# Kernel optimization log

Measured on AMD Instinct MI355X. Metric: run time of the kernel, lower is better.

The kernel has to match this reference:

```python
import jax, jax.numpy as jnp
import numpy as np
import math

B, L, D = 4, 4096, 1024
M = 256  # num random features
EPS = 1e-06


def setup_inputs() -> dict:
    key = jax.random.key(0)
    kq, kk, kv, kp = jax.random.split(key, 4)
    Q = jax.random.normal(kq, (B, L, D), dtype=jnp.float32)
    K = jax.random.normal(kk, (B, L, D), dtype=jnp.float32)
    V = jax.random.normal(kv, (B, L, D), dtype=jnp.float32)
    # Gaussian random projection (ortho_features=False path): shape (num_features, d_model)
    projection = jax.random.normal(kp, (M, D), dtype=jnp.float32)
    return {"Q": Q, "K": K, "V": V, "projection": projection}


def reference(Q, K, V, projection):
    d_model = Q.shape[-1]
    m = projection.shape[0]
    inv_sqrt_d = 1.0 / math.sqrt(d_model)
    # random features: exp((x / sqrt(d)) @ P^T)
    rf_q = jnp.exp(jnp.einsum('bld,md->blm', Q * inv_sqrt_d, projection)) / math.sqrt(m)  # (B,L,M)
    rf_k = jnp.exp(jnp.einsum('bld,md->blm', K * inv_sqrt_d, projection))                 # (B,L,M)
    # linear attention: KV state and normalizer
    KV = jnp.einsum('blm,bld->bmd', rf_k, V)   # (B,M,D)
    Z = jnp.sum(rf_k, axis=1)                   # (B,M)
    out = jnp.einsum('blm,bmd->bld', rf_q, KV)  # (B,L,D)
    normalizer = jnp.einsum('blm,bm->bl', rf_q, Z) + EPS  # (B,L)
    return out / normalizer[..., None]
```

## Files before the change

kernel.cpp:

```cpp
#include <hip/hip_runtime.h>
#include <math.h>

#define NB 4
#define LL 4096
#define DD 1024
#define MM 256

typedef short s16x8 __attribute__((ext_vector_type(8)));
typedef short s16x4 __attribute__((ext_vector_type(4)));
typedef float fx4 __attribute__((ext_vector_type(4)));
typedef unsigned u32x2 __attribute__((ext_vector_type(2)));
typedef unsigned u32x4 __attribute__((ext_vector_type(4)));

__device__ __forceinline__ float b2f(short s) {
  union { unsigned u; float f; } v;
  v.u = ((unsigned)(unsigned short)s) << 16;
  return v.f;
}
__device__ __forceinline__ short f2b(float f) {
  union { float f; unsigned u; } v;
  v.f = f;
  unsigned r = (v.u + 0x7fffu + ((v.u >> 16) & 1u)) >> 16;
  return (short)(unsigned short)r;
}
__device__ __forceinline__ unsigned cvt2(float lo, float hi) {
  unsigned r;
  asm("v_cvt_pk_bf16_f32 %0, %1, %2" : "=v"(r) : "v"(lo), "v"(hi));
  return r;
}
__device__ __forceinline__ int swz(int row, int col) {
  return row * 64 + (col ^ ((row & 7) << 3));
}
__device__ __forceinline__ int keyf(int m) { return (m ^ (m >> 2)) & 3; }

typedef __attribute__((address_space(1))) const void* gas1_t;
typedef __attribute__((address_space(3))) void* las3_t;
#define GLL16(g, l) __builtin_amdgcn_global_load_lds((gas1_t)(const void*)(g), (las3_t)(void*)(l), 16, 0, 0)

__global__ __launch_bounds__(256) void k_cast(const float* __restrict__ in, short* __restrict__ out, int n4) {
  int i = blockIdx.x * 256 + threadIdx.x;
  if (i >= n4) return;
  float4 v = ((const float4*)in)[i];
  s16x4 s;
  s[0] = f2b(v.x); s[1] = f2b(v.y); s[2] = f2b(v.z); s[3] = f2b(v.w);
  ((s16x4*)out)[i] = s;
}

__global__ __launch_bounds__(256, 2) void k_qk(const float* __restrict__ Q, const float* __restrict__ K,
                                               const short* __restrict__ Pb,
                                               short* __restrict__ rfq, short* __restrict__ rfkT,
                                               float* __restrict__ Zz) {
  __shared__ short As[2][8192];
  __shared__ short Bs[2][8192];
  int z = blockIdx.z, mode = z >> 2, b = z & 3;
  int m0 = blockIdx.x * 128, l0 = blockIdx.y * 128;
  const float* X = mode ? K : Q;
  int tid = threadIdx.x, lane = tid & 63, w = tid >> 6;
  int wr = w >> 1, wc = w & 1;
  int m16 = lane & 15, kg = lane >> 4;

  int arow = tid >> 1, acolh = (tid & 1) * 32;
  int akey = (arow & 7) << 3;
  const float* Xr = X + ((size_t)b * LL + l0 + arow) * DD + acolh;
  const short* PbB = Pb + (size_t)m0 * DD;

  fx4 acc[4][4] = {};
  float4 pa[8];

  #pragma unroll
  for (int i = 0; i < 8; ++i) pa[i] = *(const float4*)(Xr + i * 4);
  #pragma unroll
  for (int j = 0; j < 4; ++j) {
    int fl = tid + j * 256, row = fl >> 3, c8 = fl & 7;
    GLL16(PbB + (size_t)row * DD + (c8 ^ (row & 7)) * 8, &Bs[0][fl * 8]);
  }
  #pragma unroll
  for (int i = 0; i < 4; ++i) {
    u32x4 vv;
    vv[0] = cvt2(pa[2 * i].x, pa[2 * i].y);
    vv[1] = cvt2(pa[2 * i].z, pa[2 * i].w);
    vv[2] = cvt2(pa[2 * i + 1].x, pa[2 * i + 1].y);
    vv[3] = cvt2(pa[2 * i + 1].z, pa[2 * i + 1].w);
    *(u32x4*)&As[0][arow * 64 + ((acolh + i * 8) ^ akey)] = vv;
  }
  __syncthreads();

  for (int t = 0; t < 16; ++t) {
    int cur = t & 1, nxt = cur ^ 1;
    if (t < 15) {
      int d1 = (t + 1) * 64;
      #pragma unroll
      for (int i = 0; i < 8; ++i) pa[i] = *(const float4*)(Xr + d1 + i * 4);
      #pragma unroll
      for (int j = 0; j < 4; ++j) {
        int fl = tid + j * 256, row = fl >> 3, c8 = fl & 7;
        GLL16(PbB + (size_t)row * DD + d1 + (c8 ^ (row & 7)) * 8, &Bs[nxt][fl * 8]);
      }
    }
    #pragma unroll
    for (int ks = 0; ks < 2; ++ks) {
      int kb = ks * 32 + kg * 8;
      s16x8 af[4], bf[4];
      #pragma unroll
      for (int mi = 0; mi < 4; ++mi) af[mi] = *(const s16x8*)&As[cur][swz(wr * 64 + mi * 16 + m16, kb)];
      #pragma unroll
      for (int ni = 0; ni < 4; ++ni) bf[ni] = *(const s16x8*)&Bs[cur][swz(wc * 64 + ni * 16 + m16, kb)];
      #pragma unroll
      for (int mi = 0; mi < 4; ++mi)
        #pragma unroll
        for (int ni = 0; ni < 4; ++ni)
          acc[mi][ni] = __builtin_amdgcn_mfma_f32_16x16x32_bf16(af[mi], bf[ni], acc[mi][ni], 0, 0, 0);
    }
    if (t < 15) {
      #pragma unroll
      for (int i = 0; i < 4; ++i) {
        u32x4 vv;
        vv[0] = cvt2(pa[2 * i].x, pa[2 * i].y);
        vv[1] = cvt2(pa[2 * i].z, pa[2 * i].w);
        vv[2] = cvt2(pa[2 * i + 1].x, pa[2 * i + 1].y);
        vv[3] = cvt2(pa[2 * i + 1].z, pa[2 * i + 1].w);
        *(u32x4*)&As[nxt][arow * 64 + ((acolh + i * 8) ^ akey)] = vv;
      }
    }
    __syncthreads();
  }

  if (mode == 0) {
    #pragma unroll
    for (int mi = 0; mi < 4; ++mi)
      #pragma unroll
      for (int ni = 0; ni < 4; ++ni) {
        int r0 = wr * 64 + mi * 16 + (kg << 2);
        int c = m0 + wc * 64 + ni * 16 + m16;
        #pragma unroll
        for (int u = 0; u < 4; ++u)
          rfq[((size_t)b * LL + l0 + r0 + u) * MM + c] = f2b(expf(acc[mi][ni][u] * 0.03125f) * 0.0625f);
      }
  } else {
    short* T = (short*)As;
    float zp[4] = {0.f, 0.f, 0.f, 0.f};
    #pragma unroll
    for (int mi = 0; mi < 4; ++mi)
      #pragma unroll
      for (int ni = 0; ni < 4; ++ni) {
        int l = wr * 64 + mi * 16 + (kg << 2);
        int m = wc * 64 + ni * 16 + m16;
        int key = (m & 7) << 3;
        float e0 = expf(acc[mi][ni][0] * 0.03125f);
        float e1 = expf(acc[mi][ni][1] * 0.03125f);
        float e2 = expf(acc[mi][ni][2] * 0.03125f);
        float e3 = expf(acc[mi][ni][3] * 0.03125f);
        zp[ni] += e0 + e1 + e2 + e3;
        *(unsigned*)&T[m * 128 + (l ^ key)] = cvt2(e0, e1);
        *(unsigned*)&T[m * 128 + ((l + 2) ^ key)] = cvt2(e2, e3);
      }
    #pragma unroll
    for (int ni = 0; ni < 4; ++ni) {
      zp[ni] += __shfl_xor(zp[ni], 16);
      zp[ni] += __shfl_xor(zp[ni], 32);
    }
    if (kg == 0) {
      #pragma unroll
      for (int ni = 0; ni < 4; ++ni)
        atomicAdd(&Zz[b * MM + m0 + wc * 64 + ni * 16 + m16], zp[ni]);
    }
    __syncthreads();
    int m = tid >> 1, lh = (tid & 1) * 64;
    int mkey = (m & 7) << 3;
    short* dst = rfkT + ((size_t)b * MM + m0 + m) * LL + l0 + lh;
    #pragma unroll
    for (int j = 0; j < 8; ++j) {
      int l = lh + j * 8;
      s16x8 v = *(const s16x8*)&T[m * 128 + (l ^ mkey)];
      *(s16x8*)(dst + j * 8) = v;
    }
  }
}

__global__ __launch_bounds__(512) void k_kv(const float* __restrict__ V, const short* __restrict__ rfkT,
                                            float* __restrict__ KVp) {
  __shared__ float Vs[2][32 * 129];
  __shared__ short Ak[2][256 * 32];
  int d0 = blockIdx.x * 128, kc = blockIdx.y, b = blockIdx.z;
  int ls = kc * 512;
  int tid = threadIdx.x, lane = tid & 63, w = tid >> 6;
  int wm = w >> 1, wd = w & 1;
  int m16 = lane & 15, kg = lane >> 4;

  int vl = tid >> 4, vf = (tid & 15) * 8;
  const float* Vb = V + ((size_t)b * LL + ls + vl) * DD + d0 + vf;

  int am = tid >> 2, as = tid & 3;
  int acs = as ^ keyf(am);
  const short* AkS0 = rfkT + ((size_t)b * MM + am) * LL + ls + acs * 8;
  const short* AkS1 = rfkT + ((size_t)b * MM + am + 128) * LL + ls + acs * 8;

  fx4 acc[4][4] = {};
  float4 pv0, pv1;

  pv0 = *(const float4*)(Vb);
  pv1 = *(const float4*)(Vb + 4);
  GLL16(AkS0, &Ak[0][tid * 8]);
  GLL16(AkS1, &Ak[0][(tid + 512) * 8]);
  #pragma unroll
  for (int j = 0; j < 4; ++j) {
    Vs[0][vl * 129 + vf + j] = ((const float*)&pv0)[j];
    Vs[0][vl * 129 + vf + 4 + j] = ((const float*)&pv1)[j];
  }
  __syncthreads();

  for (int ch = 0; ch < 16; ++ch) {
    int cur = ch & 1, nxt = cur ^ 1;
    if (ch < 15) {
      int lo = (ch + 1) * 32;
      pv0 = *(const float4*)(Vb + (size_t)lo * DD);
      pv1 = *(const float4*)(Vb + (size_t)lo * DD + 4);
      GLL16(AkS0 + lo, &Ak[nxt][tid * 8]);
      GLL16(AkS1 + lo, &Ak[nxt][(tid + 512) * 8]);
    }
    s16x8 af[4];
    #pragma unroll
    for (int mi = 0; mi < 4; ++mi) {
      int m = wm * 64 + mi * 16 + m16;
      af[mi] = *(const s16x8*)&Ak[cur][m * 32 + ((kg ^ keyf(m)) * 8)];
    }
    #pragma unroll
    for (int ni = 0; ni < 4; ++ni) {
      int d = wd * 64 + ni * 16 + m16;
      const float* vs = &Vs[cur][kg * 8 * 129 + d];
      u32x4 bw;
      bw[0] = cvt2(vs[0], vs[129]);
      bw[1] = cvt2(vs[258], vs[387]);
      bw[2] = cvt2(vs[516], vs[645]);
      bw[3] = cvt2(vs[774], vs[903]);
      s16x8 bf = *(s16x8*)&bw;
      #pragma unroll
      for (int mi = 0; mi < 4; ++mi)
        acc[mi][ni] = __builtin_amdgcn_mfma_f32_16x16x32_bf16(af[mi], bf, acc[mi][ni], 0, 0, 0);
    }
    if (ch < 15) {
      #pragma unroll
      for (int j = 0; j < 4; ++j) {
        Vs[nxt][vl * 129 + vf + j] = ((const float*)&pv0)[j];
        Vs[nxt][vl * 129 + vf + 4 + j] = ((const float*)&pv1)[j];
      }
    }
    __syncthreads();
  }

  float* dst = KVp + (((size_t)kc * NB + b) * DD + d0) * MM;
  #pragma unroll
  for (int mi = 0; mi < 4; ++mi)
    #pragma unroll
    for (int ni = 0; ni < 4; ++ni) {
      int d = wd * 64 + ni * 16 + m16;
      int m = wm * 64 + mi * 16 + (kg << 2);
      *(float4*)(dst + (size_t)d * MM + m) = *(float4*)&acc[mi][ni];
    }
}

__global__ __launch_bounds__(256) void k_red(const float* __restrict__ KVp, float* __restrict__ KVTf) {
  int i = blockIdx.x * 256 + threadIdx.x;
  const float4* p = (const float4*)KVp;
  float4 s = p[i];
  #pragma unroll
  for (int k = 1; k < 8; ++k) {
    float4 v = p[i + k * 262144];
    s.x += v.x; s.y += v.y; s.z += v.z; s.w += v.w;
  }
  ((float4*)KVTf)[i] = s;
}

__global__ __launch_bounds__(512) void k_out(const short* __restrict__ rfq, const float* __restrict__ KVTf,
                                             const float* __restrict__ Zz, float* __restrict__ out) {
  __shared__ short Aq[2][8192];
  __shared__ short Bv[2][8192];
  __shared__ float zl[256];
  __shared__ float np[512];
  __shared__ float nf[128];
  int l0 = blockIdx.x * 128, d0 = blockIdx.y * 128, b = blockIdx.z;
  int tid = threadIdx.x, lane = tid & 63, w = tid >> 6;
  int wr = w >> 2, wc = w & 3;
  int brow = tid >> 2, bq = (tid & 3) * 16;
  int bkey = (brow & 7) << 3;
  const float* Kf = KVTf + ((size_t)b * DD + d0 + brow) * MM + bq;
  short* Bw0 = &Bv[0][brow * 64 + (bq ^ bkey)];
  short* Bw1 = &Bv[0][brow * 64 + ((bq + 8) ^ bkey)];
  const short* Ab = rfq + ((size_t)b * LL + l0) * MM;
  int f1 = tid + 512;
  int ar0 = tid >> 3, ac0 = tid & 7, ar1 = f1 >> 3, ac1 = f1 & 7;
  int nrow = tid & 127, nsub = tid >> 7;
  if (tid < 256) zl[tid] = Zz[b * MM + tid];
  fx4 acc[4][2] = {};
  float4 pb[4];
  float na = 0.f;

  #pragma unroll
  for (int i = 0; i < 4; ++i) pb[i] = *(const float4*)(Kf + i * 4);
  GLL16(Ab + (size_t)ar0 * MM + (ac0 ^ (ar0 & 7)) * 8, &Aq[0][tid * 8]);
  GLL16(Ab + (size_t)ar1 * MM + (ac1 ^ (ar1 & 7)) * 8, &Aq[0][f1 * 8]);
  {
    u32x2 v0, v1;
    v0[0] = cvt2(pb[0].x, pb[0].y); v0[1] = cvt2(pb[0].z, pb[0].w);
    v1[0] = cvt2(pb[1].x, pb[1].y); v1[1] = cvt2(pb[1].z, pb[1].w);
    *(u32x2*)Bw0 = v0;
    *(u32x2*)(Bw0 + 4) = v1;
    v0[0] = cvt2(pb[2].x, pb[2].y); v0[1] = cvt2(pb[2].z, pb[2].w);
    v1[0] = cvt2(pb[3].x, pb[3].y); v1[1] = cvt2(pb[3].z, pb[3].w);
    *(u32x2*)Bw1 = v0;
    *(u32x2*)(Bw1 + 4) = v1;
  }
  __syncthreads();

  for (int t = 0; t < 4; ++t) {
    int cur = t & 1, nxt = cur ^ 1;
    int m1 = ((t + 1) & 3) * 64;
    #pragma unroll
    for (int i = 0; i < 4; ++i) pb[i] = *(const float4*)(Kf + m1 + i * 4);
    GLL16(Ab + (size_t)ar0 * MM + m1 + (ac0 ^ (ar0 & 7)) * 8, &Aq[nxt][tid * 8]);
    GLL16(Ab + (size_t)ar1 * MM + m1 + (ac1 ^ (ar1 & 7)) * 8, &Aq[nxt][f1 * 8]);
    #pragma unroll
    for (int kk = 0; kk < 16; ++kk) {
      int k = nsub * 16 + kk;
      na += b2f(Aq[cur][nrow * 64 + (k ^ ((nrow & 7) << 3))]) * zl[t * 64 + k];
    }
    #pragma unroll
    for (int ks = 0; ks < 2; ++ks) {
      int kb = ks * 32 + (lane >> 4) * 8;
      s16x8 af[4], bf[2];
      #pragma unroll
      for (int mi = 0; mi < 4; ++mi) {
        int row = wr * 64 + mi * 16 + (lane & 15);
        af[mi] = *(const s16x8*)&Aq[cur][row * 64 + (kb ^ ((row & 7) << 3))];
      }
      #pragma unroll
      for (int ni = 0; ni < 2; ++ni) {
        int row = wc * 32 + ni * 16 + (lane & 15);
        bf[ni] = *(const s16x8*)&Bv[cur][row * 64 + (kb ^ ((row & 7) << 3))];
      }
      #pragma unroll
      for (int mi = 0; mi < 4; ++mi)
        #pragma unroll
        for (int ni = 0; ni < 2; ++ni)
          acc[mi][ni] = __builtin_amdgcn_mfma_f32_16x16x32_bf16(af[mi], bf[ni], acc[mi][ni], 0, 0, 0);
    }
    {
      u32x2 v0, v1;
      v0[0] = cvt2(pb[0].x, pb[0].y); v0[1] = cvt2(pb[0].z, pb[0].w);
      v1[0] = cvt2(pb[1].x, pb[1].y); v1[1] = cvt2(pb[1].z, pb[1].w);
      *(u32x2*)(Bw0 + nxt * 8192) = v0;
      *(u32x2*)(Bw0 + nxt * 8192 + 4) = v1;
      v0[0] = cvt2(pb[2].x, pb[2].y); v0[1] = cvt2(pb[2].z, pb[2].w);
      v1[0] = cvt2(pb[3].x, pb[3].y); v1[1] = cvt2(pb[3].z, pb[3].w);
      *(u32x2*)(Bw1 + nxt * 8192) = v0;
      *(u32x2*)(Bw1 + nxt * 8192 + 4) = v1;
    }
    __syncthreads();
  }
  np[tid] = na;
  __syncthreads();
  if (tid < 128) nf[tid] = np[tid] + np[tid + 128] + np[tid + 256] + np[tid + 384] + 1e-6f;
  __syncthreads();
  #pragma unroll
  for (int mi = 0; mi < 4; ++mi)
    #pragma unroll
    for (int ni = 0; ni < 2; ++ni) {
      int l = wr * 64 + mi * 16 + ((lane >> 4) << 2);
      int d = d0 + wc * 32 + ni * 16 + (lane & 15);
      #pragma unroll
      for (int u = 0; u < 4; ++u)
        out[((size_t)b * LL + l0 + l + u) * DD + d] = acc[mi][ni][u] / nf[l + u];
    }
}

extern "C" void kernel_launch(void* const* d_in, const int* in_sizes, int n_in,
                              void* d_out, int out_size, void* d_ws, size_t ws_size,
                              hipStream_t stream) {
  const float* Q = (const float*)d_in[0];
  const float* K = (const float*)d_in[1];
  const float* V = (const float*)d_in[2];
  const float* P = (const float*)d_in[3];
  float* out = (float*)d_out;
  char* ws = (char*)d_ws;

  short* Pb   = (short*)(ws + 0);
  float* Zz   = (float*)(ws + 524288);
  float* KVTf = (float*)(ws + 528384);
  short* rfq  = (short*)(ws + 4722688);
  short* rfkT = (short*)(ws + 13111296);
  float* KVp  = (float*)(ws + 21499904);

  k_cast<<<256, 256, 0, stream>>>(P, Pb, 65536);
  (void)hipMemsetAsync(Zz, 0, 4096, stream);
  k_qk<<<dim3(2, 32, 2 * NB), 256, 0, stream>>>(Q, K, Pb, rfq, rfkT, Zz);
  k_kv<<<dim3(8, 8, NB), 512, 0, stream>>>(V, rfkT, KVp);
  k_red<<<1024, 256, 0, stream>>>(KVp, KVTf);
  k_out<<<dim3(32, 8, NB), 512, 0, stream>>>(rfq, KVTf, Zz, out);
}
```

Before: 152.7 us.

## Retile k_qk to cover all random features per block, loading Q/K once

Changes the k_qk tile from 128 rows × 128 features to 64 rows × all 256 features, so each block spans the full feature dimension. Each fp32 Q/K row is now read and converted to bf16 by one block instead of two. This cuts the dominant HBM traffic of the feature-map stage. In exchange, every block streams the whole bf16 projection (served from L2), and per-block LDS grows to about 80KB. The epilogue transpose of rf_k and the Z atomics are re-indexed for the new tile shape.

Result: faster. 137.4 us (-10.0%).

```diff
diff --git a/kernel.cpp b/kernel.cpp
--- a/kernel.cpp
+++ b/kernel.cpp
@@ -50,38 +50,36 @@
                                                const short* __restrict__ Pb,
                                                short* __restrict__ rfq, short* __restrict__ rfkT,
                                                float* __restrict__ Zz) {
-  __shared__ short As[2][8192];
-  __shared__ short Bs[2][8192];
+  __shared__ short As[2][4096];
+  __shared__ short Bs[2][16384];
   int z = blockIdx.z, mode = z >> 2, b = z & 3;
-  int m0 = blockIdx.x * 128, l0 = blockIdx.y * 128;
+  int l0 = blockIdx.x * 64;
   const float* X = mode ? K : Q;
   int tid = threadIdx.x, lane = tid & 63, w = tid >> 6;
-  int wr = w >> 1, wc = w & 1;
   int m16 = lane & 15, kg = lane >> 4;
 
-  int arow = tid >> 1, acolh = (tid & 1) * 32;
+  int arow = tid >> 2, acol = (tid & 3) * 16;
   int akey = (arow & 7) << 3;
-  const float* Xr = X + ((size_t)b * LL + l0 + arow) * DD + acolh;
-  const short* PbB = Pb + (size_t)m0 * DD;
+  const float* Xr = X + ((size_t)b * LL + l0 + arow) * DD + acol;
 
   fx4 acc[4][4] = {};
-  float4 pa[8];
-
-  #pragma unroll
-  for (int i = 0; i < 8; ++i) pa[i] = *(const float4*)(Xr + i * 4);
-  #pragma unroll
-  for (int j = 0; j < 4; ++j) {
+  float4 pa[4];
+
+  #pragma unroll
+  for (int i = 0; i < 4; ++i) pa[i] = *(const float4*)(Xr + i * 4);
+  #pragma unroll
+  for (int j = 0; j < 8; ++j) {
     int fl = tid + j * 256, row = fl >> 3, c8 = fl & 7;
-    GLL16(PbB + (size_t)row * DD + (c8 ^ (row & 7)) * 8, &Bs[0][fl * 8]);
-  }
-  #pragma unroll
-  for (int i = 0; i < 4; ++i) {
-    u32x4 vv;
-    vv[0] = cvt2(pa[2 * i].x, pa[2 * i].y);
-    vv[1] = cvt2(pa[2 * i].z, pa[2 * i].w);
-    vv[2] = cvt2(pa[2 * i + 1].x, pa[2 * i + 1].y);
-    vv[3] = cvt2(pa[2 * i + 1].z, pa[2 * i + 1].w);
-    *(u32x4*)&As[0][arow * 64 + ((acolh + i * 8) ^ akey)] = vv;
+    GLL16(Pb + (size_t)row * DD + (c8 ^ (row & 7)) * 8, &Bs[0][fl * 8]);
+  }
+  {
+    u32x4 v0;
+    v0[0] = cvt2(pa[0].x, pa[0].y); v0[1] = cvt2(pa[0].z, pa[0].w);
+    v0[2] = cvt2(pa[1].x, pa[1].y); v0[3] = cvt2(pa[1].z, pa[1].w);
+    *(u32x4*)&As[0][arow * 64 + (acol ^ akey)] = v0;
+    v0[0] = cvt2(pa[2].x, pa[2].y); v0[1] = cvt2(pa[2].z, pa[2].w);
+    v0[2] = cvt2(pa[3].x, pa[3].y); v0[3] = cvt2(pa[3].z, pa[3].w);
+    *(u32x4*)&As[0][arow * 64 + ((acol + 8) ^ akey)] = v0;
   }
   __syncthreads();
 
@@ -90,11 +88,11 @@
     if (t < 15) {
       int d1 = (t + 1) * 64;
       #pragma unroll
-      for (int i = 0; i < 8; ++i) pa[i] = *(const float4*)(Xr + d1 + i * 4);
-      #pragma unroll
-      for (int j = 0; j < 4; ++j) {
+      for (int i = 0; i < 4; ++i) pa[i] = *(const float4*)(Xr + d1 + i * 4);
+      #pragma unroll
+      for (int j = 0; j < 8; ++j) {
         int fl = tid + j * 256, row = fl >> 3, c8 = fl & 7;
-        GLL16(PbB + (size_t)row * DD + d1 + (c8 ^ (row & 7)) * 8, &Bs[nxt][fl * 8]);
+        GLL16(Pb + (size_t)row * DD + d1 + (c8 ^ (row & 7)) * 8, &Bs[nxt][fl * 8]);
       }
     }
     #pragma unroll
@@ -102,9 +100,9 @@
       int kb = ks * 32 + kg * 8;
       s16x8 af[4], bf[4];
       #pragma unroll
-      for (int mi = 0; mi < 4; ++mi) af[mi] = *(const s16x8*)&As[cur][swz(wr * 64 + mi * 16 + m16, kb)];
-      #pragma unroll
-      for (int ni = 0; ni < 4; ++ni) bf[ni] = *(const s16x8*)&Bs[cur][swz(wc * 64 + ni * 16 + m16, kb)];
+      for (int mi = 0; mi < 4; ++mi) af[mi] = *(const s16x8*)&As[cur][swz(mi * 16 + m16, kb)];
+      #pragma unroll
+      for (int ni = 0; ni < 4; ++ni) bf[ni] = *(const s16x8*)&Bs[cur][swz(w * 64 + ni * 16 + m16, kb)];
       #pragma unroll
       for (int mi = 0; mi < 4; ++mi)
         #pragma unroll
@@ -112,15 +110,13 @@
           acc[mi][ni] = __builtin_amdgcn_mfma_f32_16x16x32_bf16(af[mi], bf[ni], acc[mi][ni], 0, 0, 0);
     }
     if (t < 15) {
-      #pragma unroll
-      for (int i = 0; i < 4; ++i) {
-        u32x4 vv;
-        vv[0] = cvt2(pa[2 * i].x, pa[2 * i].y);
-        vv[1] = cvt2(pa[2 * i].z, pa[2 * i].w);
-        vv[2] = cvt2(pa[2 * i + 1].x, pa[2 * i + 1].y);
-        vv[3] = cvt2(pa[2 * i + 1].z, pa[2 * i + 1].w);
-        *(u32x4*)&As[nxt][arow * 64 + ((acolh + i * 8) ^ akey)] = vv;
-      }
+      u32x4 v0;
+      v0[0] = cvt2(pa[0].x, pa[0].y); v0[1] = cvt2(pa[0].z, pa[0].w);
+      v0[2] = cvt2(pa[1].x, pa[1].y); v0[3] = cvt2(pa[1].z, pa[1].w);
+      *(u32x4*)&As[nxt][arow * 64 + (acol ^ akey)] = v0;
+      v0[0] = cvt2(pa[2].x, pa[2].y); v0[1] = cvt2(pa[2].z, pa[2].w);
+      v0[2] = cvt2(pa[3].x, pa[3].y); v0[3] = cvt2(pa[3].z, pa[3].w);
+      *(u32x4*)&As[nxt][arow * 64 + ((acol + 8) ^ akey)] = v0;
     }
     __syncthreads();
   }
@@ -130,29 +126,29 @@
     for (int mi = 0; mi < 4; ++mi)
       #pragma unroll
       for (int ni = 0; ni < 4; ++ni) {
-        int r0 = wr * 64 + mi * 16 + (kg << 2);
-        int c = m0 + wc * 64 + ni * 16 + m16;
+        int r0 = mi * 16 + (kg << 2);
+        int c = w * 64 + ni * 16 + m16;
         #pragma unroll
         for (int u = 0; u < 4; ++u)
           rfq[((size_t)b * LL + l0 + r0 + u) * MM + c] = f2b(expf(acc[mi][ni][u] * 0.03125f) * 0.0625f);
       }
   } else {
-    short* T = (short*)As;
+    short* T = (short*)Bs;
     float zp[4] = {0.f, 0.f, 0.f, 0.f};
     #pragma unroll
     for (int mi = 0; mi < 4; ++mi)
       #pragma unroll
       for (int ni = 0; ni < 4; ++ni) {
-        int l = wr * 64 + mi * 16 + (kg << 2);
-        int m = wc * 64 + ni * 16 + m16;
+        int l = mi * 16 + (kg << 2);
+        int m = w * 64 + ni * 16 + m16;
         int key = (m & 7) << 3;
         float e0 = expf(acc[mi][ni][0] * 0.03125f);
         float e1 = expf(acc[mi][ni][1] * 0.03125f);
         float e2 = expf(acc[mi][ni][2] * 0.03125f);
         float e3 = expf(acc[mi][ni][3] * 0.03125f);
         zp[ni] += e0 + e1 + e2 + e3;
-        *(unsigned*)&T[m * 128 + (l ^ key)] = cvt2(e0, e1);
-        *(unsigned*)&T[m * 128 + ((l + 2) ^ key)] = cvt2(e2, e3);
+        *(unsigned*)&T[m * 64 + (l ^ key)] = cvt2(e0, e1);
+        *(unsigned*)&T[m * 64 + ((l ^ key) + 2)] = cvt2(e2, e3);
       }
     #pragma unroll
     for (int ni = 0; ni < 4; ++ni) {
@@ -162,16 +158,14 @@
     if (kg == 0) {
       #pragma unroll
       for (int ni = 0; ni < 4; ++ni)
-        atomicAdd(&Zz[b * MM + m0 + wc * 64 + ni * 16 + m16], zp[ni]);
+        atomicAdd(&Zz[b * MM + w * 64 + ni * 16 + m16], zp[ni]);
     }
     __syncthreads();
-    int m = tid >> 1, lh = (tid & 1) * 64;
-    int mkey = (m & 7) << 3;
-    short* dst = rfkT + ((size_t)b * MM + m0 + m) * LL + l0 + lh;
+    int m = tid, mkey = (m & 7) << 3;
+    short* dst = rfkT + ((size_t)b * MM + m) * LL + l0;
     #pragma unroll
     for (int j = 0; j < 8; ++j) {
-      int l = lh + j * 8;
-      s16x8 v = *(const s16x8*)&T[m * 128 + (l ^ mkey)];
+      s16x8 v = *(const s16x8*)&T[m * 64 + ((j * 8) ^ mkey)];
       *(s16x8*)(dst + j * 8) = v;
     }
   }
@@ -392,7 +386,7 @@
 
   k_cast<<<256, 256, 0, stream>>>(P, Pb, 65536);
   (void)hipMemsetAsync(Zz, 0, 4096, stream);
-  k_qk<<<dim3(2, 32, 2 * NB), 256, 0, stream>>>(Q, K, Pb, rfq, rfkT, Zz);
+  k_qk<<<dim3(64, 1, 2 * NB), 256, 0, stream>>>(Q, K, Pb, rfq, rfkT, Zz);
   k_kv<<<dim3(8, 8, NB), 512, 0, stream>>>(V, rfkT, KVp);
   k_red<<<1024, 256, 0, stream>>>(KVp, KVTf);
   k_out<<<dim3(32, 8, NB), 512, 0, stream>>>(rfq, KVTf, Zz, out);
```
